# Kernel optimization log

Measured on AMD Instinct MI355X. Metric: run time of the kernel, lower is better.

Reference implementation:

```python
import jax, jax.numpy as jnp
import numpy as np

B, S, H, DH = 1, 4096, 8, 40  # hardcoded in the original forward
D = H * DH  # 320

def setup_inputs() -> dict:
    key = jax.random.key(0)
    ks = jax.random.split(key, 6)
    s = 1.0 / np.sqrt(D)
    return {
        "x": jax.random.normal(ks[0], (B, S, D), dtype=jnp.float32),
        "Wq": jax.random.normal(ks[1], (D, D), dtype=jnp.float32) * s,
        "Wk": jax.random.normal(ks[2], (D, D), dtype=jnp.float32) * s,
        "Wv": jax.random.normal(ks[3], (D, D), dtype=jnp.float32) * s,
        "Wo": jax.random.normal(ks[4], (D, D), dtype=jnp.float32) * s,
        "bo": jnp.zeros((D,), dtype=jnp.float32),
    }

def reference(x, Wq, Wk, Wv, Wo, bo):
    scale = DH ** (-0.5)
    # nn.Linear(bias=False): y = x @ W^T. context = x (self-attention).
    q = x @ Wq.T
    k = x @ Wk.T
    v = x @ Wv.T
    # split heads: [B,S,D] -> [B*H, S, DH]
    def split_heads(t):
        return t.reshape(B, S, H, DH).transpose(0, 2, 1, 3).reshape(B * H, S, DH)
    q, k, v = split_heads(q), split_heads(k), split_heads(v)
    # fp32 QK^T (original forces float), softmax, AV
    sim = jnp.einsum('bid,bjd->bij', q.astype(jnp.float32), k.astype(jnp.float32)) * scale
    attn = jax.nn.softmax(sim, axis=-1)
    out = jnp.einsum('bij,bjd->bid', attn, v)
    # merge heads: [B*H, S, DH] -> [B, S, D]
    out = out.reshape(B, H, S, DH).transpose(0, 2, 1, 3).reshape(B, S, D)
    return out @ Wo.T + bo
```

## Files before the change

### kernel.cpp

```cpp
#include <hip/hip_runtime.h>
#include <math.h>


#define NS 4096
#define ND 320
#define SCALE2 0.2281101152f
#define HS48 196608
#define VTH 163840
#define XN 1310720

#define KSTR 56
#define VSTR 72
#define VB   3584
#define BUF  7040

typedef __attribute__((ext_vector_type(8))) short bf16x8;
typedef __attribute__((ext_vector_type(16))) float f32x16;

static __device__ __forceinline__ unsigned short f2bru(float f) {
  return (unsigned short)((__builtin_bit_cast(unsigned int, f) + 0x8000u) >> 16);
}
static __device__ __forceinline__ unsigned int pk2ru(float a, float b) {
  unsigned int ua = __builtin_bit_cast(unsigned int, a) + 0x8000u;
  unsigned int ub = __builtin_bit_cast(unsigned int, b) + 0x8000u;
  return __builtin_amdgcn_perm(ub, ua, 0x07060302u);
}
static __device__ __forceinline__ unsigned int pk2t(float a, float b) {
  return __builtin_amdgcn_perm(__builtin_bit_cast(unsigned int, b),
                               __builtin_bit_cast(unsigned int, a), 0x07060302u);
}
static __device__ __forceinline__ float fexp2(float x) {
  return __builtin_amdgcn_exp2f(x);
}
static __device__ __forceinline__ bf16x8 ld8a(const unsigned short* p) {
  return __builtin_bit_cast(bf16x8, *(const uint4*)p);
}
static __device__ __forceinline__ void st16a(unsigned short* p, uint4 v) {
  *(uint4*)p = v;
}
static __device__ __forceinline__ uint4 ld16u(const unsigned short* p) {
  uint2 a = *(const uint2*)p, b = *(const uint2*)(p + 4);
  return make_uint4(a.x, a.y, b.x, b.y);
}
static __device__ __forceinline__ void st16(unsigned short* p, uint4 v) {
  *(uint2*)p = make_uint2(v.x, v.y);
  *(uint2*)(p + 4) = make_uint2(v.z, v.w);
}
static __device__ __forceinline__ int sig32(int q) {
  int s = q >> 4, h2 = (q >> 3) & 1, j = q & 7;
  return (s << 4) | ((j >> 2) << 3) | (h2 << 2) | (j & 3);
}

__global__ __launch_bounds__(256) void proj_qkv_kernel(
    const float* __restrict__ x, const float* __restrict__ Wq,
    const float* __restrict__ Wk, const float* __restrict__ Wv,
    unsigned short* __restrict__ Qp, unsigned short* __restrict__ Kp,
    unsigned short* __restrict__ Vt) {
  const int zi = blockIdx.y;
  const int z = zi / 5;
  const int bnn = (zi - z * 5) * 64;
  const float* W = (z == 0) ? Wq : (z == 1) ? Wk : Wv;
  __shared__ __align__(16) unsigned short As[2][64 * 88];
  __shared__ __align__(16) unsigned short Bs[2][64 * 88];
  const int t = threadIdx.x;
  const int w = t >> 6, l = t & 63, l31 = l & 31, hi = l >> 5;
  const int bm = blockIdx.x * 64;
  const int m0 = (w >> 1) * 32, n0 = (w & 1) * 32;
  f32x16 acc = {0,0,0,0,0,0,0,0,0,0,0,0,0,0,0,0};
  const int afo = (m0 + l31) * 88 + hi * 8;
  const int bfo = (n0 + l31) * 88 + hi * 8;
  const int row0 = t >> 3, row1 = row0 + 32, kc = (t & 7) << 3;
  const float* xb = x + (bm + row0) * ND + kc;
  const float* xb1 = x + (bm + row1) * ND + kc;
  const float* Wb = W + (bnn + row0) * ND + kc;
  const float* Wb1 = W + (bnn + row1) * ND + kc;
  const int so0 = row0 * 88 + kc, so1 = row1 * 88 + kc;

  float4 a00, a01, a10, a11, b00, b01, b10, b11;
#define PQ_LOAD(K)                                                   \
  do {                                                               \
    a00 = *(const float4*)(xb + (K));  a01 = *(const float4*)(xb + (K) + 4);  \
    a10 = *(const float4*)(xb1 + (K)); a11 = *(const float4*)(xb1 + (K) + 4); \
    b00 = *(const float4*)(Wb + (K));  b01 = *(const float4*)(Wb + (K) + 4);  \
    b10 = *(const float4*)(Wb1 + (K)); b11 = *(const float4*)(Wb1 + (K) + 4); \
  } while (0)
#define PQ_STORE(BUFI)                                               \
  do {                                                               \
    st16a(&As[BUFI][so0], make_uint4(pk2ru(a00.x, a00.y), pk2ru(a00.z, a00.w), \
                                     pk2ru(a01.x, a01.y), pk2ru(a01.z, a01.w))); \
    st16a(&As[BUFI][so1], make_uint4(pk2ru(a10.x, a10.y), pk2ru(a10.z, a10.w), \
                                     pk2ru(a11.x, a11.y), pk2ru(a11.z, a11.w))); \
    st16a(&Bs[BUFI][so0], make_uint4(pk2ru(b00.x, b00.y), pk2ru(b00.z, b00.w), \
                                     pk2ru(b01.x, b01.y), pk2ru(b01.z, b01.w))); \
    st16a(&Bs[BUFI][so1], make_uint4(pk2ru(b10.x, b10.y), pk2ru(b10.z, b10.w), \
                                     pk2ru(b11.x, b11.y), pk2ru(b11.z, b11.w))); \
  } while (0)

  PQ_LOAD(0);
  PQ_STORE(0);
  PQ_LOAD(64);
  __syncthreads();
#pragma unroll
  for (int it = 0; it < 5; ++it) {
    const int cur = it & 1, nxt = cur ^ 1;
    if (it < 4) PQ_STORE(nxt);
    {
      int kp = (it + 2) * 64;
      if (kp >= ND) kp = 0;
      PQ_LOAD(kp);
    }
#pragma unroll
    for (int kk = 0; kk < 4; kk++) {
      acc = __builtin_amdgcn_mfma_f32_32x32x16_bf16(
          ld8a(&As[cur][afo + kk * 16]), ld8a(&Bs[cur][bfo + kk * 16]), acc, 0, 0, 0);
    }
    __syncthreads();
  }
#undef PQ_LOAD
#undef PQ_STORE

  unsigned short* Tile = &As[0][0];
  if (z < 2) {
    unsigned short* Y = (z == 0) ? Qp : Kp;
    const float sc = (z == 0) ? SCALE2 : 1.0f;
    const unsigned int padw = (z == 0) ? 0xC200u : 0x3F80u;
#pragma unroll
    for (int r2 = 0; r2 < 16; r2++) {
      int lr = m0 + (r2 & 3) + 8 * (r2 >> 2) + 4 * hi;
      Tile[lr * 68 + n0 + l31] = f2bru(acc[r2] * sc);
    }
    __syncthreads();
#pragma unroll
    for (int i = 0; i < 2; i++) {
      int c = t + i * 256;
      int row = c >> 3, ch = c & 7;
      int j = bnn + ch * 8;
      int h = j / 40, dh = j - h * 40;
      uint4 v = ld16u(Tile + row * 68 + ch * 8);
      st16(Y + h * HS48 + (bm + row) * 48 + dh, v);
      if (dh == 0)
        st16(Y + h * HS48 + (bm + row) * 48 + 40, make_uint4(padw, 0u, 0u, 0u));
    }
  } else {
#pragma unroll
    for (int r2 = 0; r2 < 16; r2++) {
      int lr = m0 + (r2 & 3) + 8 * (r2 >> 2) + 4 * hi;
      Tile[(n0 + l31) * 68 + lr] = f2bru(acc[r2]);
    }
    __syncthreads();
#pragma unroll
    for (int i = 0; i < 2; i++) {
      int c = t + i * 256;
      int row = c >> 3, ch = c & 7;
      int j = bnn + row;
      int h = j / 40, dd = j - h * 40;
      uint4 v = ld16u(Tile + row * 68 + ch * 8);
      st16(Vt + h * VTH + dd * NS + bm + ch * 8, v);
    }
  }
}

__global__ __launch_bounds__(256, 4) void attn_kernel(
    const unsigned short* __restrict__ Qp, const unsigned short* __restrict__ Kp,
    const unsigned short* __restrict__ Vt, unsigned short* __restrict__ Op,
    float* __restrict__ Lp) {
  const int b = blockIdx.x;
  const int h = b & 7, ks = (b >> 3) & 1, qt = b >> 4;
  const int t = threadIdx.x;
  const int w = t >> 6, l = t & 63, l31 = l & 31, hi = l >> 5;
  __shared__ __align__(16) unsigned short Lds[2 * BUF];
  for (int i = t; i < 576; i += 256) {
    int bsel = (i >= 288) ? 1 : 0;
    int ui = i - bsel * 288;
    int rr = ui / 36, cc = ui - rr * 36;
    ((unsigned int*)Lds)[bsel * (BUF / 2) + (VB / 2) + (40 + rr) * 36 + cc] =
        (rr == 0 && cc < 32) ? 0x3F803F80u : 0u;
  }

  const int kbase = ks * 2048;
  const int qbase = qt * 128 + w * 32;
  const unsigned short* qp = Qp + h * HS48 + (qbase + l31) * 48 + hi * 8;
  bf16x8 qf0 = *(const bf16x8*)qp;
  bf16x8 qf1 = *(const bf16x8*)(qp + 16);
  bf16x8 qf2 = *(const bf16x8*)(qp + 32);

  const f32x16 Z = {0,0,0,0,0,0,0,0,0,0,0,0,0,0,0,0};
  f32x16 oa0 = Z, oa1 = Z;

  const int id1 = t + 256;
  const bool has2 = (t < 192);
  const int kr0 = t / 6, kc0 = t - kr0 * 6;
  const unsigned short* g0 = Kp + h * HS48 + (kbase + kr0) * 48 + kc0 * 8;
  const int w0 = ((kr0 & 32) | sig32(kr0 & 31)) * KSTR + kc0 * 8;
  const unsigned short* g1;
  int w1, inc1;
  if (id1 < 384) {
    int kr = id1 / 6, kc = id1 - kr * 6;
    g1 = Kp + h * HS48 + (kbase + kr) * 48 + kc * 8;
    w1 = ((kr & 32) | sig32(kr & 31)) * KSTR + kc * 8;
    inc1 = 64 * 48;
  } else {
    int vid = id1 - 384, vr = vid >> 3, vc = vid & 7;
    g1 = Vt + h * VTH + vr * NS + kbase + vc * 8;
    w1 = VB + vr * VSTR + vc * 8;
    inc1 = 64;
  }
  const int vid2 = t + 128;
  const int vr2 = vid2 >> 3, vc2 = vid2 & 7;
  const unsigned short* g2 = Vt + h * VTH + vr2 * NS + kbase + vc2 * 8;
  const int w2 = VB + vr2 * VSTR + vc2 * 8;

  const int rk  = l31 * KSTR + hi * 8;
  const int rv0 = VB + l31 * VSTR + hi * 8;
  const int rv1 = VB + (32 + (l31 & 15)) * VSTR + hi * 8;

  uint4 r0 = *(const uint4*)g0; g0 += 3072;
  uint4 r1 = *(const uint4*)g1; g1 += inc1;
  uint4 r2{};
  if (has2) { r2 = *(const uint4*)g2; g2 += 64; }
  st16a(Lds + w0, r0);
  st16a(Lds + w1, r1);
  if (has2) st16a(Lds + w2, r2);
  r0 = *(const uint4*)g0; g0 += 3072;
  r1 = *(const uint4*)g1; g1 += inc1;
  if (has2) { r2 = *(const uint4*)g2; g2 += 64; }
  __syncthreads();

  for (int it = 0; it < 32; ++it) {
    const int bo = (it & 1) ? BUF : 0;
    const int bn = BUF - bo;
    st16a(Lds + bn + w0, r0);
    st16a(Lds + bn + w1, r1);
    if (has2) st16a(Lds + bn + w2, r2);
    r0 = *(const uint4*)g0; g0 += 3072;
    r1 = *(const uint4*)g1; g1 += inc1;
    if (has2) { r2 = *(const uint4*)g2; g2 += 64; }

    const unsigned short* kf0 = Lds + bo + rk;
    const unsigned short* kf1 = kf0 + 32 * KSTR;
    const unsigned short* vf0 = Lds + bo + rv0;
    const unsigned short* vf1 = Lds + bo + rv1;

    __builtin_amdgcn_s_setprio(1);
    {
      f32x16 s0 = __builtin_amdgcn_mfma_f32_32x32x16_bf16(ld8a(kf0), qf0, Z, 0, 0, 0);
      s0 = __builtin_amdgcn_mfma_f32_32x32x16_bf16(ld8a(kf0 + 16), qf1, s0, 0, 0, 0);
      s0 = __builtin_amdgcn_mfma_f32_32x32x16_bf16(ld8a(kf0 + 32), qf2, s0, 0, 0, 0);
      unsigned int pw[8];
#pragma unroll
      for (int i = 0; i < 8; i++)
        pw[i] = pk2t(fexp2(s0[2 * i]), fexp2(s0[2 * i + 1]));
      bf16x8 pf0 = __builtin_bit_cast(bf16x8, make_uint4(pw[0], pw[1], pw[2], pw[3]));
      bf16x8 pf1 = __builtin_bit_cast(bf16x8, make_uint4(pw[4], pw[5], pw[6], pw[7]));
      oa0 = __builtin_amdgcn_mfma_f32_32x32x16_bf16(pf0, ld8a(vf0), oa0, 0, 0, 0);
      oa1 = __builtin_amdgcn_mfma_f32_32x32x16_bf16(pf0, ld8a(vf1), oa1, 0, 0, 0);
      oa0 = __builtin_amdgcn_mfma_f32_32x32x16_bf16(pf1, ld8a(vf0 + 16), oa0, 0, 0, 0);
      oa1 = __builtin_amdgcn_mfma_f32_32x32x16_bf16(pf1, ld8a(vf1 + 16), oa1, 0, 0, 0);
    }
    {
      f32x16 s1 = __builtin_amdgcn_mfma_f32_32x32x16_bf16(ld8a(kf1), qf0, Z, 0, 0, 0);
      s1 = __builtin_amdgcn_mfma_f32_32x32x16_bf16(ld8a(kf1 + 16), qf1, s1, 0, 0, 0);
      s1 = __builtin_amdgcn_mfma_f32_32x32x16_bf16(ld8a(kf1 + 32), qf2, s1, 0, 0, 0);
      unsigned int pw[8];
#pragma unroll
      for (int i = 0; i < 8; i++)
        pw[i] = pk2t(fexp2(s1[2 * i]), fexp2(s1[2 * i + 1]));
      bf16x8 pf2 = __builtin_bit_cast(bf16x8, make_uint4(pw[0], pw[1], pw[2], pw[3]));
      bf16x8 pf3 = __builtin_bit_cast(bf16x8, make_uint4(pw[4], pw[5], pw[6], pw[7]));
      oa0 = __builtin_amdgcn_mfma_f32_32x32x16_bf16(pf2, ld8a(vf0 + 32), oa0, 0, 0, 0);
      oa1 = __builtin_amdgcn_mfma_f32_32x32x16_bf16(pf2, ld8a(vf1 + 32), oa1, 0, 0, 0);
      oa0 = __builtin_amdgcn_mfma_f32_32x32x16_bf16(pf3, ld8a(vf0 + 48), oa0, 0, 0, 0);
      oa1 = __builtin_amdgcn_mfma_f32_32x32x16_bf16(pf3, ld8a(vf1 + 48), oa1, 0, 0, 0);
    }
    __builtin_amdgcn_s_setprio(0);
    __syncthreads();
  }

  unsigned short* opb = Op + ks * XN + h * 163840;
  float* lpb = Lp + ks * 32768 + h * NS;
#pragma unroll
  for (int r2i = 0; r2i < 16; r2i++) {
    int qr = qbase + (r2i & 3) + 8 * (r2i >> 2) + 4 * hi;
    opb[qr * 40 + l31] = f2bru(oa0[r2i]);
    if (l31 < 8) opb[qr * 40 + 32 + l31] = f2bru(oa1[r2i]);
    if (l31 == 8) lpb[qr] = oa1[r2i];
  }
}

__global__ __launch_bounds__(256) void combine_kernel(
    const unsigned short* __restrict__ Op, const float* __restrict__ Lp,
    unsigned short* __restrict__ Xo) {
  int e = (blockIdx.x * 256 + threadIdx.x) * 8;
  int h = e / 163840;
  int r = e - h * 163840;
  int s = r / 40;
  int dh = r - s * 40;
  float a[8] = {0, 0, 0, 0, 0, 0, 0, 0};
  float lsum = 0.f;
#pragma unroll
  for (int k = 0; k < 2; k++) {
    uint4 u = *(const uint4*)(Op + k * XN + e);
    a[0] += __builtin_bit_cast(float, u.x << 16);
    a[1] += __builtin_bit_cast(float, u.x & 0xFFFF0000u);
    a[2] += __builtin_bit_cast(float, u.y << 16);
    a[3] += __builtin_bit_cast(float, u.y & 0xFFFF0000u);
    a[4] += __builtin_bit_cast(float, u.z << 16);
    a[5] += __builtin_bit_cast(float, u.z & 0xFFFF0000u);
    a[6] += __builtin_bit_cast(float, u.w << 16);
    a[7] += __builtin_bit_cast(float, u.w & 0xFFFF0000u);
    lsum += Lp[k * 32768 + h * NS + s];
  }
  float inv = 1.0f / lsum;
  *(uint4*)(Xo + s * ND + h * 40 + dh) =
      make_uint4(pk2ru(a[0] * inv, a[1] * inv), pk2ru(a[2] * inv, a[3] * inv),
                 pk2ru(a[4] * inv, a[5] * inv), pk2ru(a[6] * inv, a[7] * inv));
}

__global__ __launch_bounds__(256) void proj_out_kernel(
    const unsigned short* __restrict__ Xo, const float* __restrict__ Wo,
    const float* __restrict__ bo, float* __restrict__ out) {
  __shared__ __align__(16) unsigned short As[64 * 88];
  __shared__ __align__(16) unsigned short Bs[64 * 88];
  const int t = threadIdx.x;
  const int w = t >> 6, l = t & 63, l31 = l & 31, hi = l >> 5;
  const int bm = blockIdx.x * 64;
  const int bnn = blockIdx.y * 64;
  const int m0 = (w >> 1) * 32, n0 = (w & 1) * 32;
  f32x16 acc = {0,0,0,0,0,0,0,0,0,0,0,0,0,0,0,0};
  const unsigned short* af = As + (m0 + l31) * 88 + hi * 8;
  const unsigned short* bf = Bs + (n0 + l31) * 88 + hi * 8;
  for (int k0 = 0; k0 < ND; k0 += 64) {
    __syncthreads();
#pragma unroll
    for (int i = 0; i < 2; i++) {
      int c = t + i * 256;
      int row = c >> 3, kc = (c & 7) << 3;
      uint4 v = *(const uint4*)(Xo + (bm + row) * ND + k0 + kc);
      st16a(As + row * 88 + kc, v);
    }
#pragma unroll
    for (int i = 0; i < 2; i++) {
      int c = t + i * 256;
      int row = c >> 3, kc = (c & 7) << 3;
      const float* g = Wo + (bnn + row) * ND + k0 + kc;
      float4 v0 = *(const float4*)g, v1 = *(const float4*)(g + 4);
      st16a(Bs + row * 88 + kc,
            make_uint4(pk2ru(v0.x, v0.y), pk2ru(v0.z, v0.w),
                       pk2ru(v1.x, v1.y), pk2ru(v1.z, v1.w)));
    }
    __syncthreads();
#pragma unroll
    for (int ks = 0; ks < 4; ks++) {
      acc = __builtin_amdgcn_mfma_f32_32x32x16_bf16(
          ld8a(af + ks * 16), ld8a(bf + ks * 16), acc, 0, 0, 0);
    }
  }
  const int j = bnn + n0 + l31;
  const float bj = bo[j];
#pragma unroll
  for (int r2 = 0; r2 < 16; r2++) {
    int row = bm + m0 + (r2 & 3) + 8 * (r2 >> 2) + 4 * hi;
    out[row * ND + j] = acc[r2] + bj;
  }
}

extern "C" void kernel_launch(void* const* d_in, const int* in_sizes, int n_in,
                              void* d_out, int out_size, void* d_ws, size_t ws_size,
                              hipStream_t stream) {
  (void)in_sizes; (void)n_in; (void)out_size; (void)ws_size;
  const float* x  = (const float*)d_in[0];
  const float* Wq = (const float*)d_in[1];
  const float* Wk = (const float*)d_in[2];
  const float* Wv = (const float*)d_in[3];
  const float* Wo = (const float*)d_in[4];
  const float* bo = (const float*)d_in[5];
  float* out = (float*)d_out;

  unsigned short* Qp = (unsigned short*)d_ws;
  unsigned short* Kp = Qp + 8 * HS48;
  unsigned short* Vt = Kp + 8 * HS48;
  unsigned short* Xo = Vt + 8 * VTH;
  unsigned short* Op = Xo + XN;
  float* Lp = (float*)(Op + 2 * XN);

  proj_qkv_kernel<<<dim3(64, 15), 256, 0, stream>>>(x, Wq, Wk, Wv, Qp, Kp, Vt);
  attn_kernel<<<dim3(512), 256, 0, stream>>>(Qp, Kp, Vt, Op, Lp);
  combine_kernel<<<dim3(640), 256, 0, stream>>>(Op, Lp, Xo);
  proj_out_kernel<<<dim3(64, 5), 256, 0, stream>>>(Xo, Wo, bo, out);
}
```

Before: 119.3 us.

## Pre-convert inputs to bf16 and fuse split-K combine into attention via atomic counter

A new prep kernel converts x and all four weight matrices to bf16 once, so the projection kernels load half as many bytes and skip repeated fp32-to-bf16 packing (x was reconverted 15 times across the QKV grid). The separate combine kernel is removed: each attention block bumps a per-(head, q-tile) atomic counter, and the second of the two split-K blocks merges both partial outputs, normalises and writes Xo. This trades one launch and a pass over Op for an extra kernel, a fence-based handshake and extra workspace.

```diff
diff --git a/kernel.cpp b/kernel.cpp
--- a/kernel.cpp
+++ b/kernel.cpp
@@ -8,6 +8,7 @@
 #define HS48 196608
 #define VTH 163840
 #define XN 1310720
+#define WN 102400
 
 #define KSTR 56
 #define VSTR 72
@@ -51,15 +52,41 @@
   return (s << 4) | ((j >> 2) << 3) | (h2 << 2) | (j & 3);
 }
 
-__global__ __launch_bounds__(256) void proj_qkv_kernel(
+__global__ __launch_bounds__(256) void prep_kernel(
     const float* __restrict__ x, const float* __restrict__ Wq,
     const float* __restrict__ Wk, const float* __restrict__ Wv,
+    const float* __restrict__ Wo, unsigned short* __restrict__ Xb,
+    unsigned short* __restrict__ Wqb, unsigned short* __restrict__ Wkb,
+    unsigned short* __restrict__ Wvb, unsigned short* __restrict__ Wob,
+    int* __restrict__ Cnt) {
+  int idx = (blockIdx.x * 256 + threadIdx.x) * 8;
+  const float* src;
+  unsigned short* dst;
+  int off;
+  if (idx < XN) {
+    src = x; dst = Xb; off = idx;
+  } else {
+    int r = idx - XN;
+    int wsel = r / WN;
+    off = r - wsel * WN;
+    src = (wsel == 0) ? Wq : (wsel == 1) ? Wk : (wsel == 2) ? Wv : Wo;
+    dst = (wsel == 0) ? Wqb : (wsel == 1) ? Wkb : (wsel == 2) ? Wvb : Wob;
+  }
+  float4 v0 = *(const float4*)(src + off), v1 = *(const float4*)(src + off + 4);
+  *(uint4*)(dst + off) = make_uint4(pk2ru(v0.x, v0.y), pk2ru(v0.z, v0.w),
+                                    pk2ru(v1.x, v1.y), pk2ru(v1.z, v1.w));
+  if (blockIdx.x == 0) Cnt[threadIdx.x] = 0;
+}
+
+__global__ __launch_bounds__(256) void proj_qkv_kernel(
+    const unsigned short* __restrict__ Xb, const unsigned short* __restrict__ Wqb,
+    const unsigned short* __restrict__ Wkb, const unsigned short* __restrict__ Wvb,
     unsigned short* __restrict__ Qp, unsigned short* __restrict__ Kp,
     unsigned short* __restrict__ Vt) {
   const int zi = blockIdx.y;
   const int z = zi / 5;
   const int bnn = (zi - z * 5) * 64;
-  const float* W = (z == 0) ? Wq : (z == 1) ? Wk : Wv;
+  const unsigned short* W = (z == 0) ? Wqb : (z == 1) ? Wkb : Wvb;
   __shared__ __align__(16) unsigned short As[2][64 * 88];
   __shared__ __align__(16) unsigned short Bs[2][64 * 88];
   const int t = threadIdx.x;
@@ -70,30 +97,26 @@
   const int afo = (m0 + l31) * 88 + hi * 8;
   const int bfo = (n0 + l31) * 88 + hi * 8;
   const int row0 = t >> 3, row1 = row0 + 32, kc = (t & 7) << 3;
-  const float* xb = x + (bm + row0) * ND + kc;
-  const float* xb1 = x + (bm + row1) * ND + kc;
-  const float* Wb = W + (bnn + row0) * ND + kc;
-  const float* Wb1 = W + (bnn + row1) * ND + kc;
+  const unsigned short* xb = Xb + (bm + row0) * ND + kc;
+  const unsigned short* xb1 = Xb + (bm + row1) * ND + kc;
+  const unsigned short* Wb = W + (bnn + row0) * ND + kc;
+  const unsigned short* Wb1 = W + (bnn + row1) * ND + kc;
   const int so0 = row0 * 88 + kc, so1 = row1 * 88 + kc;
 
-  float4 a00, a01, a10, a11, b00, b01, b10, b11;
-#define PQ_LOAD(K)                                                   \
-  do {                                                               \
-    a00 = *(const float4*)(xb + (K));  a01 = *(const float4*)(xb + (K) + 4);  \
-    a10 = *(const float4*)(xb1 + (K)); a11 = *(const float4*)(xb1 + (K) + 4); \
-    b00 = *(const float4*)(Wb + (K));  b01 = *(const float4*)(Wb + (K) + 4);  \
-    b10 = *(const float4*)(Wb1 + (K)); b11 = *(const float4*)(Wb1 + (K) + 4); \
+  uint4 a0v, a1v, b0v, b1v;
+#define PQ_LOAD(K)                              \
+  do {                                          \
+    a0v = *(const uint4*)(xb + (K));            \
+    a1v = *(const uint4*)(xb1 + (K));           \
+    b0v = *(const uint4*)(Wb + (K));            \
+    b1v = *(const uint4*)(Wb1 + (K));           \
   } while (0)
-#define PQ_STORE(BUFI)                                               \
-  do {                                                               \
-    st16a(&As[BUFI][so0], make_uint4(pk2ru(a00.x, a00.y), pk2ru(a00.z, a00.w), \
-                                     pk2ru(a01.x, a01.y), pk2ru(a01.z, a01.w))); \
-    st16a(&As[BUFI][so1], make_uint4(pk2ru(a10.x, a10.y), pk2ru(a10.z, a10.w), \
-                                     pk2ru(a11.x, a11.y), pk2ru(a11.z, a11.w))); \
-    st16a(&Bs[BUFI][so0], make_uint4(pk2ru(b00.x, b00.y), pk2ru(b00.z, b00.w), \
-                                     pk2ru(b01.x, b01.y), pk2ru(b01.z, b01.w))); \
-    st16a(&Bs[BUFI][so1], make_uint4(pk2ru(b10.x, b10.y), pk2ru(b10.z, b10.w), \
-                                     pk2ru(b11.x, b11.y), pk2ru(b11.z, b11.w))); \
+#define PQ_STORE(BUFI)                          \
+  do {                                          \
+    st16a(&As[BUFI][so0], a0v);                 \
+    st16a(&As[BUFI][so1], a1v);                 \
+    st16a(&Bs[BUFI][so0], b0v);                 \
+    st16a(&Bs[BUFI][so1], b1v);                 \
   } while (0)
 
   PQ_LOAD(0);
@@ -163,12 +186,14 @@
 __global__ __launch_bounds__(256, 4) void attn_kernel(
     const unsigned short* __restrict__ Qp, const unsigned short* __restrict__ Kp,
     const unsigned short* __restrict__ Vt, unsigned short* __restrict__ Op,
-    float* __restrict__ Lp) {
+    float* __restrict__ Lp, unsigned short* __restrict__ Xo,
+    int* __restrict__ Cnt) {
   const int b = blockIdx.x;
   const int h = b & 7, ks = (b >> 3) & 1, qt = b >> 4;
   const int t = threadIdx.x;
   const int w = t >> 6, l = t & 63, l31 = l & 31, hi = l >> 5;
   __shared__ __align__(16) unsigned short Lds[2 * BUF];
+  __shared__ int smFlag;
   for (int i = t; i < 576; i += 256) {
     int bsel = (i >= 288) ? 1 : 0;
     int ui = i - bsel * 288;
@@ -285,39 +310,35 @@
     if (l31 < 8) opb[qr * 40 + 32 + l31] = f2bru(oa1[r2i]);
     if (l31 == 8) lpb[qr] = oa1[r2i];
   }
-}
-
-__global__ __launch_bounds__(256) void combine_kernel(
-    const unsigned short* __restrict__ Op, const float* __restrict__ Lp,
-    unsigned short* __restrict__ Xo) {
-  int e = (blockIdx.x * 256 + threadIdx.x) * 8;
-  int h = e / 163840;
-  int r = e - h * 163840;
-  int s = r / 40;
-  int dh = r - s * 40;
-  float a[8] = {0, 0, 0, 0, 0, 0, 0, 0};
-  float lsum = 0.f;
-#pragma unroll
-  for (int k = 0; k < 2; k++) {
-    uint4 u = *(const uint4*)(Op + k * XN + e);
-    a[0] += __builtin_bit_cast(float, u.x << 16);
-    a[1] += __builtin_bit_cast(float, u.x & 0xFFFF0000u);
-    a[2] += __builtin_bit_cast(float, u.y << 16);
-    a[3] += __builtin_bit_cast(float, u.y & 0xFFFF0000u);
-    a[4] += __builtin_bit_cast(float, u.z << 16);
-    a[5] += __builtin_bit_cast(float, u.z & 0xFFFF0000u);
-    a[6] += __builtin_bit_cast(float, u.w << 16);
-    a[7] += __builtin_bit_cast(float, u.w & 0xFFFF0000u);
-    lsum += Lp[k * 32768 + h * NS + s];
-  }
-  float inv = 1.0f / lsum;
-  *(uint4*)(Xo + s * ND + h * 40 + dh) =
-      make_uint4(pk2ru(a[0] * inv, a[1] * inv), pk2ru(a[2] * inv, a[3] * inv),
-                 pk2ru(a[4] * inv, a[5] * inv), pk2ru(a[6] * inv, a[7] * inv));
+
+  __syncthreads();
+  if (t == 0) {
+    __threadfence();
+    smFlag = atomicAdd(&Cnt[h * 32 + qt], 1);
+  }
+  __syncthreads();
+  if (smFlag == 0) return;
+  __threadfence();
+  const int base = h * 163840 + qt * 5120;
+  for (int i = t; i < 2560; i += 256) {
+    int i2 = i * 2;
+    int r = i2 / 40;
+    int dh = i2 - r * 40;
+    int s = qt * 128 + r;
+    float lsum = Lp[h * NS + s] + Lp[32768 + h * NS + s];
+    float inv = 1.0f / lsum;
+    unsigned int u0 = *(const unsigned int*)(Op + base + i2);
+    unsigned int u1 = *(const unsigned int*)(Op + XN + base + i2);
+    float a0 = __builtin_bit_cast(float, u0 << 16) +
+               __builtin_bit_cast(float, u1 << 16);
+    float a1 = __builtin_bit_cast(float, u0 & 0xFFFF0000u) +
+               __builtin_bit_cast(float, u1 & 0xFFFF0000u);
+    *(unsigned int*)(Xo + s * ND + h * 40 + dh) = pk2ru(a0 * inv, a1 * inv);
+  }
 }
 
 __global__ __launch_bounds__(256) void proj_out_kernel(
-    const unsigned short* __restrict__ Xo, const float* __restrict__ Wo,
+    const unsigned short* __restrict__ Xo, const unsigned short* __restrict__ Wob,
     const float* __restrict__ bo, float* __restrict__ out) {
   __shared__ __align__(16) unsigned short As[64 * 88];
   __shared__ __align__(16) unsigned short Bs[64 * 88];
@@ -342,11 +363,8 @@
     for (int i = 0; i < 2; i++) {
       int c = t + i * 256;
       int row = c >> 3, kc = (c & 7) << 3;
-      const float* g = Wo + (bnn + row) * ND + k0 + kc;
-      float4 v0 = *(const float4*)g, v1 = *(const float4*)(g + 4);
-      st16a(Bs + row * 88 + kc,
-            make_uint4(pk2ru(v0.x, v0.y), pk2ru(v0.z, v0.w),
-                       pk2ru(v1.x, v1.y), pk2ru(v1.z, v1.w)));
+      uint4 v = *(const uint4*)(Wob + (bnn + row) * ND + k0 + kc);
+      st16a(Bs + row * 88 + kc, v);
     }
     __syncthreads();
 #pragma unroll
@@ -382,9 +400,17 @@
   unsigned short* Xo = Vt + 8 * VTH;
   unsigned short* Op = Xo + XN;
   float* Lp = (float*)(Op + 2 * XN);
-
-  proj_qkv_kernel<<<dim3(64, 15), 256, 0, stream>>>(x, Wq, Wk, Wv, Qp, Kp, Vt);
-  attn_kernel<<<dim3(512), 256, 0, stream>>>(Qp, Kp, Vt, Op, Lp);
-  combine_kernel<<<dim3(640), 256, 0, stream>>>(Op, Lp, Xo);
-  proj_out_kernel<<<dim3(64, 5), 256, 0, stream>>>(Xo, Wo, bo, out);
-}
+  unsigned short* Xb = (unsigned short*)(Lp + 65536);
+  unsigned short* Wqb = Xb + XN;
+  unsigned short* Wkb = Wqb + WN;
+  unsigned short* Wvb = Wkb + WN;
+  unsigned short* Wob = Wvb + WN;
+  int* Cnt = (int*)(Wob + WN);
+
+  prep_kernel<<<dim3(840), 256, 0, stream>>>(x, Wq, Wk, Wv, Wo,
+                                             Xb, Wqb, Wkb, Wvb, Wob, Cnt);
+  proj_qkv_kernel<<<dim3(64, 15), 256, 0, stream>>>(Xb, Wqb, Wkb, Wvb,
+                                                    Qp, Kp, Vt);
+  attn_kernel<<<dim3(512), 256, 0, stream>>>(Qp, Kp, Vt, Op, Lp, Xo, Cnt);
+  proj_out_kernel<<<dim3(64, 5), 256, 0, stream>>>(Xo, Wob, bo, out);
+}
```

After: 160.7 us. 34.7% more time.

## Fuse split-K combine into attention kernel via in-block LDS reduction

Applied to the files above, without the earlier changes.

Each attention block now runs 512 threads, with two 256-thread groups each handling one half of the key range for the same query tile. The two partial outputs are reduced through shared memory and normalized by the row sum in the block, which writes the final bf16 Xo directly. This drops the separate combine kernel launch, the global round-trip of bf16 partials and row sums, and one rounding step. In exchange the grid halves to 256 blocks, each with double the LDS and a final barrier-coupled reduction, which may reduce occupancy or latency hiding.

```diff
diff --git a/kernel.cpp b/kernel.cpp
--- a/kernel.cpp
+++ b/kernel.cpp
@@ -160,24 +160,27 @@
   }
 }
 
-__global__ __launch_bounds__(256, 4) void attn_kernel(
+__global__ __launch_bounds__(512, 2) void attn_kernel(
     const unsigned short* __restrict__ Qp, const unsigned short* __restrict__ Kp,
-    const unsigned short* __restrict__ Vt, unsigned short* __restrict__ Op,
-    float* __restrict__ Lp) {
+    const unsigned short* __restrict__ Vt, unsigned short* __restrict__ Xo) {
   const int b = blockIdx.x;
-  const int h = b & 7, ks = (b >> 3) & 1, qt = b >> 4;
+  const int h = b & 7, qt = b >> 3;
   const int t = threadIdx.x;
-  const int w = t >> 6, l = t & 63, l31 = l & 31, hi = l >> 5;
-  __shared__ __align__(16) unsigned short Lds[2 * BUF];
-  for (int i = t; i < 576; i += 256) {
+  const int g = t >> 8;
+  const int lt = t & 255;
+  const int w = lt >> 6;
+  const int l = t & 63, l31 = l & 31, hi = l >> 5;
+  __shared__ __align__(16) unsigned short Lds[4 * BUF];
+  unsigned short* gl = Lds + g * (2 * BUF);
+  for (int i = lt; i < 576; i += 256) {
     int bsel = (i >= 288) ? 1 : 0;
     int ui = i - bsel * 288;
     int rr = ui / 36, cc = ui - rr * 36;
-    ((unsigned int*)Lds)[bsel * (BUF / 2) + (VB / 2) + (40 + rr) * 36 + cc] =
+    ((unsigned int*)gl)[bsel * (BUF / 2) + (VB / 2) + (40 + rr) * 36 + cc] =
         (rr == 0 && cc < 32) ? 0x3F803F80u : 0u;
   }
 
-  const int kbase = ks * 2048;
+  const int kbase = g * 2048;
   const int qbase = qt * 128 + w * 32;
   const unsigned short* qp = Qp + h * HS48 + (qbase + l31) * 48 + hi * 8;
   bf16x8 qf0 = *(const bf16x8*)qp;
@@ -187,9 +190,9 @@
   const f32x16 Z = {0,0,0,0,0,0,0,0,0,0,0,0,0,0,0,0};
   f32x16 oa0 = Z, oa1 = Z;
 
-  const int id1 = t + 256;
-  const bool has2 = (t < 192);
-  const int kr0 = t / 6, kc0 = t - kr0 * 6;
+  const int id1 = lt + 256;
+  const bool has2 = (lt < 192);
+  const int kr0 = lt / 6, kc0 = lt - kr0 * 6;
   const unsigned short* g0 = Kp + h * HS48 + (kbase + kr0) * 48 + kc0 * 8;
   const int w0 = ((kr0 & 32) | sig32(kr0 & 31)) * KSTR + kc0 * 8;
   const unsigned short* g1;
@@ -205,7 +208,7 @@
     w1 = VB + vr * VSTR + vc * 8;
     inc1 = 64;
   }
-  const int vid2 = t + 128;
+  const int vid2 = lt + 128;
   const int vr2 = vid2 >> 3, vc2 = vid2 & 7;
   const unsigned short* g2 = Vt + h * VTH + vr2 * NS + kbase + vc2 * 8;
   const int w2 = VB + vr2 * VSTR + vc2 * 8;
@@ -218,9 +221,9 @@
   uint4 r1 = *(const uint4*)g1; g1 += inc1;
   uint4 r2{};
   if (has2) { r2 = *(const uint4*)g2; g2 += 64; }
-  st16a(Lds + w0, r0);
-  st16a(Lds + w1, r1);
-  if (has2) st16a(Lds + w2, r2);
+  st16a(gl + w0, r0);
+  st16a(gl + w1, r1);
+  if (has2) st16a(gl + w2, r2);
   r0 = *(const uint4*)g0; g0 += 3072;
   r1 = *(const uint4*)g1; g1 += inc1;
   if (has2) { r2 = *(const uint4*)g2; g2 += 64; }
@@ -229,17 +232,17 @@
   for (int it = 0; it < 32; ++it) {
     const int bo = (it & 1) ? BUF : 0;
     const int bn = BUF - bo;
-    st16a(Lds + bn + w0, r0);
-    st16a(Lds + bn + w1, r1);
-    if (has2) st16a(Lds + bn + w2, r2);
+    st16a(gl + bn + w0, r0);
+    st16a(gl + bn + w1, r1);
+    if (has2) st16a(gl + bn + w2, r2);
     r0 = *(const uint4*)g0; g0 += 3072;
     r1 = *(const uint4*)g1; g1 += inc1;
     if (has2) { r2 = *(const uint4*)g2; g2 += 64; }
 
-    const unsigned short* kf0 = Lds + bo + rk;
+    const unsigned short* kf0 = gl + bo + rk;
     const unsigned short* kf1 = kf0 + 32 * KSTR;
-    const unsigned short* vf0 = Lds + bo + rv0;
-    const unsigned short* vf1 = Lds + bo + rv1;
+    const unsigned short* vf0 = gl + bo + rv0;
+    const unsigned short* vf1 = gl + bo + rv1;
 
     __builtin_amdgcn_s_setprio(1);
     {
@@ -276,44 +279,32 @@
     __syncthreads();
   }
 
-  unsigned short* opb = Op + ks * XN + h * 163840;
-  float* lpb = Lp + ks * 32768 + h * NS;
-#pragma unroll
-  for (int r2i = 0; r2i < 16; r2i++) {
-    int qr = qbase + (r2i & 3) + 8 * (r2i >> 2) + 4 * hi;
-    opb[qr * 40 + l31] = f2bru(oa0[r2i]);
-    if (l31 < 8) opb[qr * 40 + 32 + l31] = f2bru(oa1[r2i]);
-    if (l31 == 8) lpb[qr] = oa1[r2i];
-  }
-}
-
-__global__ __launch_bounds__(256) void combine_kernel(
-    const unsigned short* __restrict__ Op, const float* __restrict__ Lp,
-    unsigned short* __restrict__ Xo) {
-  int e = (blockIdx.x * 256 + threadIdx.x) * 8;
-  int h = e / 163840;
-  int r = e - h * 163840;
-  int s = r / 40;
-  int dh = r - s * 40;
-  float a[8] = {0, 0, 0, 0, 0, 0, 0, 0};
-  float lsum = 0.f;
-#pragma unroll
-  for (int k = 0; k < 2; k++) {
-    uint4 u = *(const uint4*)(Op + k * XN + e);
-    a[0] += __builtin_bit_cast(float, u.x << 16);
-    a[1] += __builtin_bit_cast(float, u.x & 0xFFFF0000u);
-    a[2] += __builtin_bit_cast(float, u.y << 16);
-    a[3] += __builtin_bit_cast(float, u.y & 0xFFFF0000u);
-    a[4] += __builtin_bit_cast(float, u.z << 16);
-    a[5] += __builtin_bit_cast(float, u.z & 0xFFFF0000u);
-    a[6] += __builtin_bit_cast(float, u.w << 16);
-    a[7] += __builtin_bit_cast(float, u.w & 0xFFFF0000u);
-    lsum += Lp[k * 32768 + h * NS + s];
-  }
-  float inv = 1.0f / lsum;
-  *(uint4*)(Xo + s * ND + h * 40 + dh) =
-      make_uint4(pk2ru(a[0] * inv, a[1] * inv), pk2ru(a[2] * inv, a[3] * inv),
-                 pk2ru(a[4] * inv, a[5] * inv), pk2ru(a[6] * inv, a[7] * inv));
+  float* fl = (float*)Lds;
+  const int slot = (w * 64 + l) * 32;
+  if (g == 1) {
+#pragma unroll
+    for (int i = 0; i < 16; i++) {
+      fl[slot + i] = oa0[i];
+      fl[slot + 16 + i] = oa1[i];
+    }
+  }
+  __syncthreads();
+  if (g == 0) {
+#pragma unroll
+    for (int i = 0; i < 16; i++) {
+      oa0[i] += fl[slot + i];
+      oa1[i] += fl[slot + 16 + i];
+    }
+    const int srcl = (l & 32) | 8;
+#pragma unroll
+    for (int r2i = 0; r2i < 16; r2i++) {
+      int qr = qbase + (r2i & 3) + 8 * (r2i >> 2) + 4 * hi;
+      float ls = __shfl(oa1[r2i], srcl);
+      float inv = 1.0f / ls;
+      Xo[qr * ND + h * 40 + l31] = f2bru(oa0[r2i] * inv);
+      if (l31 < 8) Xo[qr * ND + h * 40 + 32 + l31] = f2bru(oa1[r2i] * inv);
+    }
+  }
 }
 
 __global__ __launch_bounds__(256) void proj_out_kernel(
@@ -342,8 +333,8 @@
     for (int i = 0; i < 2; i++) {
       int c = t + i * 256;
       int row = c >> 3, kc = (c & 7) << 3;
-      const float* g = Wo + (bnn + row) * ND + k0 + kc;
-      float4 v0 = *(const float4*)g, v1 = *(const float4*)(g + 4);
+      const float* gp = Wo + (bnn + row) * ND + k0 + kc;
+      float4 v0 = *(const float4*)gp, v1 = *(const float4*)(gp + 4);
       st16a(Bs + row * 88 + kc,
             make_uint4(pk2ru(v0.x, v0.y), pk2ru(v0.z, v0.w),
                        pk2ru(v1.x, v1.y), pk2ru(v1.z, v1.w)));
@@ -380,11 +371,8 @@
   unsigned short* Kp = Qp + 8 * HS48;
   unsigned short* Vt = Kp + 8 * HS48;
   unsigned short* Xo = Vt + 8 * VTH;
-  unsigned short* Op = Xo + XN;
-  float* Lp = (float*)(Op + 2 * XN);
 
   proj_qkv_kernel<<<dim3(64, 15), 256, 0, stream>>>(x, Wq, Wk, Wv, Qp, Kp, Vt);
-  attn_kernel<<<dim3(512), 256, 0, stream>>>(Qp, Kp, Vt, Op, Lp);
-  combine_kernel<<<dim3(640), 256, 0, stream>>>(Op, Lp, Xo);
+  attn_kernel<<<dim3(256), 512, 0, stream>>>(Qp, Kp, Vt, Xo);
   proj_out_kernel<<<dim3(64, 5), 256, 0, stream>>>(Xo, Wo, bo, out);
 }
```

Measured after the change: 118.5 us (median of 2 runs). No clear change (-0.6%).
